# Performance work log

Measured on AMD Instinct MI355X. Metric: run time of the kernel, lower is better.

The kernel has to match this reference:

```python
import jax, jax.numpy as jnp
import numpy as np

B, T, E = 4, 2048, 1024
H, KV = 16, 4          # query heads, key/value heads
D = E // H             # head_dim = 64
G = H // KV            # query heads per kv head = 4
NEG = -1e9


def setup_inputs() -> dict:
    key = jax.random.key(0)
    ks = jax.random.split(key, 6)
    hidden_states = jax.random.normal(ks[0], (B, T, E), dtype=jnp.float32)
    # additive causal mask [B, 1, T, T]
    causal = jnp.where(jnp.tril(jnp.ones((T, T), dtype=bool)), 0.0, NEG).astype(jnp.float32)
    attention_mask = jnp.broadcast_to(causal[None, None], (B, 1, T, T))
    s = 0.02
    Wq = jax.random.normal(ks[1], (E, E), dtype=jnp.float32) * s
    Wk = jax.random.normal(ks[2], (E, KV * D), dtype=jnp.float32) * s
    Wv = jax.random.normal(ks[3], (E, KV * D), dtype=jnp.float32) * s
    Wo = jax.random.normal(ks[4], (E, E), dtype=jnp.float32) * s
    bq = jnp.zeros((E,), jnp.float32)
    bk = jnp.zeros((KV * D,), jnp.float32)
    bv = jnp.zeros((KV * D,), jnp.float32)
    bo = jnp.zeros((E,), jnp.float32)
    return {"hidden_states": hidden_states, "attention_mask": attention_mask,
            "Wq": Wq, "bq": bq, "Wk": Wk, "bk": bk, "Wv": Wv, "bv": bv,
            "Wo": Wo, "bo": bo}


def reference(hidden_states, attention_mask, Wq, bq, Wk, bk, Wv, bv, Wo, bo):
    b, t, e = hidden_states.shape
    scaling = D ** -0.5
    # projections (torch Linear: x @ W + b with W stored [in, out])
    q = (hidden_states @ Wq + bq) * scaling           # [b, t, E]
    k = hidden_states @ Wk + bk                        # [b, t, KV*D]
    v = hidden_states @ Wv + bv
    # [b, KV, G, t, D] for q; [b, KV, t, D] for k/v (GQA grouping == repeat_kv math)
    q = q.reshape(b, t, KV, G, D).transpose(0, 2, 3, 1, 4)
    k = k.reshape(b, t, KV, D).transpose(0, 2, 1, 3)
    v = v.reshape(b, t, KV, D).transpose(0, 2, 1, 3)
    scores = jnp.einsum('bkgsd,bktd->bkgst', q, k)     # [b, KV, G, t, t]
    scores = scores + attention_mask[:, :, None, :, :]  # broadcast [b,1,1,t,t]
    w = jax.nn.softmax(scores, axis=-1)
    out = jnp.einsum('bkgst,bktd->bkgsd', w, v)        # [b, KV, G, t, D]
    out = out.transpose(0, 3, 1, 2, 4).reshape(b, t, e)  # heads back to embed
    return out @ Wo + bo
```

## Files before the change

### kernel.cpp

```cpp
#include <hip/hip_runtime.h>

typedef __bf16 bf16;
typedef __attribute__((ext_vector_type(8))) __bf16 bf16x8;
typedef __attribute__((ext_vector_type(4))) __bf16 bf16x4;
typedef __attribute__((ext_vector_type(4))) float f32x4;

#define B_ 4
#define T_ 2048
#define E_ 1024
#define H_ 16
#define KV_ 4
#define D_ 64
#define KVD_ 256
#define KVSTRIDE_ 512
#define M_ 8192

#define MASK_NEG (-3.0e4f)

__device__ inline bf16x8 load8(const bf16* p) { return *(const bf16x8*)p; }
__device__ inline bf16x8 load8(const float* p) {
  f32x4 a = *(const f32x4*)p;
  f32x4 b = *(const f32x4*)(p + 4);
  bf16x8 r;
#pragma unroll
  for (int j = 0; j < 4; ++j) { r[j] = (bf16)a[j]; r[4 + j] = (bf16)b[j]; }
  return r;
}

__device__ inline void gload_lds16(const bf16* g, bf16* l) {
  __builtin_amdgcn_global_load_lds(
      (const __attribute__((address_space(1))) void*)g,
      (__attribute__((address_space(3))) void*)l, 16, 0, 0);
}

__global__ __launch_bounds__(256) void cast_k(const float* __restrict__ src,
                                              bf16* __restrict__ dst) {
  size_t i = ((size_t)blockIdx.x * 256 + threadIdx.x) * 8;
  *(bf16x8*)(dst + i) = load8(src + i);
}

__global__ __launch_bounds__(256) void transpose_k(const float* __restrict__ W,
                                                   bf16* __restrict__ WT,
                                                   int K, int N) {
  __shared__ bf16 tile[32][33];
  int k0 = blockIdx.x * 32, n0 = blockIdx.y * 32;
  int tr = threadIdx.x >> 5;
  int tc = threadIdx.x & 31;
#pragma unroll
  for (int i = 0; i < 32; i += 8)
    tile[tr + i][tc] = (bf16)W[(size_t)(k0 + tr + i) * N + n0 + tc];
  __syncthreads();
#pragma unroll
  for (int i = 0; i < 32; i += 8)
    WT[(size_t)(n0 + tr + i) * K + k0 + tc] = tile[tc][tr + i];
}

__global__ __launch_bounds__(256) void vtrans_k(const bf16* __restrict__ src,
                                                bf16* __restrict__ dst) {
  __shared__ bf16 tile[32][33];
  int r0 = blockIdx.x * 32;
  int c0 = blockIdx.y * 32;
  int tr = threadIdx.x >> 5, tc = threadIdx.x & 31;
#pragma unroll
  for (int i = 0; i < 32; i += 8)
    tile[tr + i][tc] = src[(size_t)(r0 + tr + i) * KVSTRIDE_ + 256 + c0 + tc];
  __syncthreads();
#pragma unroll
  for (int i = 0; i < 32; i += 8) {
    int c = c0 + tr + i;
    int r = r0 + tc;
    dst[(size_t)((r >> 11) * KVD_ + c) * T_ + (r & (T_ - 1))] = tile[tc][tr + i];
  }
}

template <typename CT>
__global__ __launch_bounds__(256) void gemm128_k(const bf16* __restrict__ A,
                                                 const bf16* __restrict__ WT,
                                                 const float* __restrict__ bias0,
                                                 const float* __restrict__ bias1,
                                                 int nsplit,
                                                 CT* __restrict__ C,
                                                 int M, int N, int K, float scale) {
  const int m0 = blockIdx.x * 128;
  const int n0 = blockIdx.y * 128;
  const int tid = threadIdx.x;
  const int wave = tid >> 6;
  const int lane = tid & 63;
  const int wr = wave >> 1;
  const int wc = wave & 1;
  const int fr = lane & 15;
  const int quad = lane >> 4;

  __shared__ bf16 sA[128][32];
  __shared__ bf16 sB[128][32];

  f32x4 acc[4][4] = {};

  const int ldr = lane >> 2;
  const int ldk = (lane & 3) * 8;
  const bf16* Ag0 = A + (size_t)(m0 + wave * 32 + ldr) * K + ldk;
  const bf16* Ag1 = Ag0 + (size_t)16 * K;
  const bf16* Bg0 = WT + (size_t)(n0 + wave * 32 + ldr) * K + ldk;
  const bf16* Bg1 = Bg0 + (size_t)16 * K;
  bf16* sA0 = &sA[wave * 32][0];
  bf16* sA1 = &sA[wave * 32 + 16][0];
  bf16* sB0 = &sB[wave * 32][0];
  bf16* sB1 = &sB[wave * 32 + 16][0];

  for (int k0 = 0; k0 < K; k0 += 32) {
    gload_lds16(Ag0 + k0, sA0);
    gload_lds16(Ag1 + k0, sA1);
    gload_lds16(Bg0 + k0, sB0);
    gload_lds16(Bg1 + k0, sB1);
    __syncthreads();

    bf16x8 af[4], bfr[4];
#pragma unroll
    for (int m = 0; m < 4; ++m)
      af[m] = *(const bf16x8*)(&sA[wr * 64 + m * 16 + fr][quad * 8]);
#pragma unroll
    for (int n = 0; n < 4; ++n)
      bfr[n] = *(const bf16x8*)(&sB[wc * 64 + n * 16 + fr][quad * 8]);
#pragma unroll
    for (int m = 0; m < 4; ++m)
#pragma unroll
      for (int n = 0; n < 4; ++n)
        acc[m][n] = __builtin_amdgcn_mfma_f32_16x16x32_bf16(af[m], bfr[n], acc[m][n], 0, 0, 0);
    __syncthreads();
  }

#pragma unroll
  for (int n = 0; n < 4; ++n) {
    int col = n0 + wc * 64 + n * 16 + fr;
    float bv = (col < nsplit) ? bias0[col] : bias1[col - nsplit];
#pragma unroll
    for (int m = 0; m < 4; ++m) {
#pragma unroll
      for (int i = 0; i < 4; ++i) {
        int row = m0 + wr * 64 + m * 16 + quad * 4 + i;
        C[(size_t)row * N + col] = (CT)((acc[m][n][i] + bv) * scale);
      }
    }
  }
}

__global__ __launch_bounds__(256) void attn_k(const bf16* __restrict__ Qg,
                                              const bf16* __restrict__ Kg,
                                              const bf16* __restrict__ VTg,
                                              bf16* __restrict__ Og) {
  const int jp = blockIdx.x;
  const int h = blockIdx.y;
  const int b = blockIdx.z;
  const int kv = h >> 2;
  const int tid = threadIdx.x;
  const int wave = tid >> 6;
  const int lane = tid & 63;
  const int fr = lane & 15;
  const int quad = lane >> 4;

  __shared__ bf16 Ks[64][72];
  __shared__ bf16 Vt[64][72];
  __shared__ bf16 Pt[64][72];

  const int skey = tid & 63;
  const int sdc = (tid >> 6) * 16;
  const int svd = tid >> 2;
  const int svk = (tid & 3) * 16;
  const bf16* kbase = Kg + (size_t)(b * T_ + skey) * KVSTRIDE_ + kv * 64 + sdc;
  const bf16* vbase = VTg + (size_t)((b * KV_ + kv) * D_ + svd) * T_ + svk;

  for (int ph = 0; ph < 2; ++ph) {
    const int qb = ph ? (31 - jp) : jp;

    bf16x8 qa0, qa1;
    {
      const bf16* qsrc = Qg + (size_t)(b * T_ + qb * 64 + wave * 16 + fr) * E_ + h * 64 + quad * 8;
      qa0 = *(const bf16x8*)(qsrc);
      qa1 = *(const bf16x8*)(qsrc + 32);
    }

    f32x4 Oacc[4] = {};
    float m_run = MASK_NEG, l_run = 0.f;

    bf16x8 k0p, k1p, v0p, v1p;
    k0p = *(const bf16x8*)(kbase);
    k1p = *(const bf16x8*)(kbase + 8);
    v0p = *(const bf16x8*)(vbase);
    v1p = *(const bf16x8*)(vbase + 8);

    for (int kb = 0; kb <= qb; ++kb) {
      *(bf16x8*)(&Ks[skey][sdc]) = k0p;
      *(bf16x8*)(&Ks[skey][sdc + 8]) = k1p;
      *(bf16x8*)(&Vt[svd][svk]) = v0p;
      *(bf16x8*)(&Vt[svd][svk + 8]) = v1p;
      __syncthreads();

      if (kb < qb) {
        const bf16* kp = kbase + (size_t)(kb + 1) * 64 * KVSTRIDE_;
        const bf16* vp = vbase + (size_t)(kb + 1) * 64;
        k0p = *(const bf16x8*)(kp);
        k1p = *(const bf16x8*)(kp + 8);
        v0p = *(const bf16x8*)(vp);
        v1p = *(const bf16x8*)(vp + 8);
      } else if (ph == 0) {
        k0p = *(const bf16x8*)(kbase);
        k1p = *(const bf16x8*)(kbase + 8);
        v0p = *(const bf16x8*)(vbase);
        v1p = *(const bf16x8*)(vbase + 8);
      }

      f32x4 S[4] = {};
#pragma unroll
      for (int nt = 0; nt < 4; ++nt) {
        bf16x8 kf0 = *(const bf16x8*)(&Ks[nt * 16 + fr][quad * 8]);
        bf16x8 kf1 = *(const bf16x8*)(&Ks[nt * 16 + fr][32 + quad * 8]);
        S[nt] = __builtin_amdgcn_mfma_f32_16x16x32_bf16(kf0, qa0, S[nt], 0, 0, 0);
        S[nt] = __builtin_amdgcn_mfma_f32_16x16x32_bf16(kf1, qa1, S[nt], 0, 0, 0);
      }

      if (kb == qb) {
        const int ql = wave * 16 + fr;
#pragma unroll
        for (int nt = 0; nt < 4; ++nt)
#pragma unroll
          for (int i = 0; i < 4; ++i)
            if (nt * 16 + quad * 4 + i > ql) S[nt][i] = MASK_NEG;
      }

      float pm = S[0][0];
#pragma unroll
      for (int nt = 0; nt < 4; ++nt)
#pragma unroll
        for (int i = 0; i < 4; ++i) pm = fmaxf(pm, S[nt][i]);
      pm = fmaxf(pm, __shfl_xor(pm, 16, 64));
      pm = fmaxf(pm, __shfl_xor(pm, 32, 64));
      if (pm > m_run) {
        float al = exp2f(m_run - pm);
        m_run = pm;
        l_run *= al;
#pragma unroll
        for (int dt = 0; dt < 4; ++dt)
#pragma unroll
          for (int i = 0; i < 4; ++i) Oacc[dt][i] *= al;
      }
      float ps = 0.f;
#pragma unroll
      for (int nt = 0; nt < 4; ++nt)
#pragma unroll
        for (int i = 0; i < 4; ++i) {
          float p = exp2f(S[nt][i] - m_run);
          S[nt][i] = p;
          ps += p;
        }
      ps += __shfl_xor(ps, 16, 64);
      ps += __shfl_xor(ps, 32, 64);
      l_run += ps;

#pragma unroll
      for (int nt = 0; nt < 4; ++nt) {
        bf16x4 w;
#pragma unroll
        for (int i = 0; i < 4; ++i) w[i] = (bf16)S[nt][i];
        *(bf16x4*)(&Pt[wave * 16 + fr][nt * 16 + quad * 4]) = w;
      }
      __threadfence_block();

      bf16x8 pb0 = *(const bf16x8*)(&Pt[wave * 16 + fr][quad * 8]);
      bf16x8 pb1 = *(const bf16x8*)(&Pt[wave * 16 + fr][32 + quad * 8]);
#pragma unroll
      for (int dt = 0; dt < 4; ++dt) {
        bf16x8 vf0 = *(const bf16x8*)(&Vt[dt * 16 + fr][quad * 8]);
        bf16x8 vf1 = *(const bf16x8*)(&Vt[dt * 16 + fr][32 + quad * 8]);
        Oacc[dt] = __builtin_amdgcn_mfma_f32_16x16x32_bf16(vf0, pb0, Oacc[dt], 0, 0, 0);
        Oacc[dt] = __builtin_amdgcn_mfma_f32_16x16x32_bf16(vf1, pb1, Oacc[dt], 0, 0, 0);
      }
      __syncthreads();
    }

    {
      float inv = 1.f / fmaxf(l_run, 1e-30f);
      bf16* dst = Og + (size_t)(b * T_ + qb * 64 + wave * 16 + fr) * E_ + h * 64;
#pragma unroll
      for (int dt = 0; dt < 4; ++dt) {
        bf16x4 o;
#pragma unroll
        for (int i = 0; i < 4; ++i) o[i] = (bf16)(Oacc[dt][i] * inv);
        *(bf16x4*)(dst + dt * 16 + quad * 4) = o;
      }
    }
  }
}

extern "C" void kernel_launch(void* const* d_in, const int* in_sizes, int n_in,
                              void* d_out, int out_size, void* d_ws, size_t ws_size,
                              hipStream_t stream) {
  (void)in_sizes; (void)n_in; (void)out_size; (void)ws_size;
  const float* hidden = (const float*)d_in[0];
  const float* Wq = (const float*)d_in[2];
  const float* bq = (const float*)d_in[3];
  const float* Wk = (const float*)d_in[4];
  const float* bk = (const float*)d_in[5];
  const float* Wv = (const float*)d_in[6];
  const float* bv = (const float*)d_in[7];
  const float* Wo = (const float*)d_in[8];
  const float* bo = (const float*)d_in[9];
  float* out = (float*)d_out;

  char* ws = (char*)d_ws;
  bf16* WqT  = (bf16*)(ws);
  bf16* WoT  = (bf16*)(ws + (2u << 20));
  bf16* WkvT = (bf16*)(ws + (4u << 20));
  bf16* Qb   = (bf16*)(ws + (5u << 20));
  bf16* KVb  = (bf16*)(ws + (21u << 20));
  bf16* Hb   = (bf16*)(ws + (29u << 20));
  bf16* Ab   = (bf16*)(ws + (29u << 20));
  bf16* VbT  = (bf16*)(ws + (45u << 20));

  cast_k<<<dim3(M_ * E_ / (256 * 8)), 256, 0, stream>>>(hidden, Hb);
  transpose_k<<<dim3(32, 32), 256, 0, stream>>>(Wq, WqT, 1024, 1024);
  transpose_k<<<dim3(32, 8), 256, 0, stream>>>(Wk, WkvT, 1024, 256);
  transpose_k<<<dim3(32, 8), 256, 0, stream>>>(Wv, WkvT + (256u * 1024u), 1024, 256);
  transpose_k<<<dim3(32, 32), 256, 0, stream>>>(Wo, WoT, 1024, 1024);

  gemm128_k<bf16><<<dim3(64, 8), 256, 0, stream>>>(Hb, WqT, bq, bq, 1 << 30, Qb, M_, E_, E_,
                                                   0.125f * 1.4426950408889634f);
  gemm128_k<bf16><<<dim3(64, 4), 256, 0, stream>>>(Hb, WkvT, bk, bv, 256, KVb, M_, KVSTRIDE_, E_, 1.0f);

  vtrans_k<<<dim3(256, 8), 256, 0, stream>>>(KVb, VbT);

  attn_k<<<dim3(16, 16, 4), 256, 0, stream>>>(Qb, KVb, VbT, Ab);

  gemm128_k<float><<<dim3(64, 8), 256, 0, stream>>>(Ab, WoT, bo, bo, 1 << 30, out, M_, E_, E_, 1.0f);
}
```

Before: 313.7 us.

## Fuse Q/K/V projections into one GEMM, batch weight transposes, add MFMA priority

Concatenates Wq, Wk and Wv into one transposed weight and computes Q, K and V in a single GEMM writing an interleaved QKV buffer with a 1536-column stride. The four weight transpose launches become one 3D launch. Attention and the V transpose now read from the fused buffer. The attention MFMA sections are also wrapped in s_setprio to favour matrix issue. This cuts launch count and gives better wave fill for the projections, at the cost of a wider row stride for the Q and K reads in attention.

```diff
diff --git a/kernel.cpp b/kernel.cpp
--- a/kernel.cpp
+++ b/kernel.cpp
@@ -12,10 +12,11 @@
 #define KV_ 4
 #define D_ 64
 #define KVD_ 256
-#define KVSTRIDE_ 512
+#define QKVS_ 1536
 #define M_ 8192
 
 #define MASK_NEG (-3.0e4f)
+#define QSCALE (0.125f * 1.4426950408889634f)
 
 __device__ inline bf16x8 load8(const bf16* p) { return *(const bf16x8*)p; }
 __device__ inline bf16x8 load8(const float* p) {
@@ -39,9 +40,21 @@
   *(bf16x8*)(dst + i) = load8(src + i);
 }
 
-__global__ __launch_bounds__(256) void transpose_k(const float* __restrict__ W,
-                                                   bf16* __restrict__ WT,
-                                                   int K, int N) {
+__global__ __launch_bounds__(256) void wprep_k(const float* __restrict__ Wq,
+                                               const float* __restrict__ Wk,
+                                               const float* __restrict__ Wv,
+                                               const float* __restrict__ Wo,
+                                               bf16* __restrict__ WqkvT,
+                                               bf16* __restrict__ WoT) {
+  const int z = blockIdx.z;
+  const float* W;
+  bf16* WT;
+  int N;
+  if (z == 0) { W = Wq; WT = WqkvT; N = 1024; }
+  else if (z == 1) { W = Wo; WT = WoT; N = 1024; }
+  else if (z == 2) { if (blockIdx.y >= 8) return; W = Wk; WT = WqkvT + 1024 * 1024; N = 256; }
+  else { if (blockIdx.y >= 8) return; W = Wv; WT = WqkvT + 1280 * 1024; N = 256; }
+
   __shared__ bf16 tile[32][33];
   int k0 = blockIdx.x * 32, n0 = blockIdx.y * 32;
   int tr = threadIdx.x >> 5;
@@ -52,7 +65,7 @@
   __syncthreads();
 #pragma unroll
   for (int i = 0; i < 32; i += 8)
-    WT[(size_t)(n0 + tr + i) * K + k0 + tc] = tile[tc][tr + i];
+    WT[(size_t)(n0 + tr + i) * 1024 + k0 + tc] = tile[tc][tr + i];
 }
 
 __global__ __launch_bounds__(256) void vtrans_k(const bf16* __restrict__ src,
@@ -63,7 +76,7 @@
   int tr = threadIdx.x >> 5, tc = threadIdx.x & 31;
 #pragma unroll
   for (int i = 0; i < 32; i += 8)
-    tile[tr + i][tc] = src[(size_t)(r0 + tr + i) * KVSTRIDE_ + 256 + c0 + tc];
+    tile[tr + i][tc] = src[(size_t)(r0 + tr + i) * QKVS_ + 1280 + c0 + tc];
   __syncthreads();
 #pragma unroll
   for (int i = 0; i < 32; i += 8) {
@@ -73,14 +86,13 @@
   }
 }
 
-template <typename CT>
-__global__ __launch_bounds__(256) void gemm128_k(const bf16* __restrict__ A,
-                                                 const bf16* __restrict__ WT,
-                                                 const float* __restrict__ bias0,
-                                                 const float* __restrict__ bias1,
-                                                 int nsplit,
-                                                 CT* __restrict__ C,
-                                                 int M, int N, int K, float scale) {
+__global__ __launch_bounds__(256) void qkv_gemm_k(const bf16* __restrict__ A,
+                                                  const bf16* __restrict__ WT,
+                                                  const float* __restrict__ bq,
+                                                  const float* __restrict__ bk,
+                                                  const float* __restrict__ bv,
+                                                  bf16* __restrict__ C) {
+  const int K = E_;
   const int m0 = blockIdx.x * 128;
   const int n0 = blockIdx.y * 128;
   const int tid = threadIdx.x;
@@ -132,20 +144,90 @@
 #pragma unroll
   for (int n = 0; n < 4; ++n) {
     int col = n0 + wc * 64 + n * 16 + fr;
-    float bv = (col < nsplit) ? bias0[col] : bias1[col - nsplit];
+    float bias, sc;
+    if (col < 1024) { bias = bq[col]; sc = QSCALE; }
+    else if (col < 1280) { bias = bk[col - 1024]; sc = 1.f; }
+    else { bias = bv[col - 1280]; sc = 1.f; }
 #pragma unroll
     for (int m = 0; m < 4; ++m) {
 #pragma unroll
       for (int i = 0; i < 4; ++i) {
         int row = m0 + wr * 64 + m * 16 + quad * 4 + i;
-        C[(size_t)row * N + col] = (CT)((acc[m][n][i] + bv) * scale);
+        C[(size_t)row * QKVS_ + col] = (bf16)((acc[m][n][i] + bias) * sc);
       }
     }
   }
 }
 
-__global__ __launch_bounds__(256) void attn_k(const bf16* __restrict__ Qg,
-                                              const bf16* __restrict__ Kg,
+__global__ __launch_bounds__(256) void gemm128_k(const bf16* __restrict__ A,
+                                                 const bf16* __restrict__ WT,
+                                                 const float* __restrict__ bias,
+                                                 float* __restrict__ C,
+                                                 int M, int N, int K) {
+  const int m0 = blockIdx.x * 128;
+  const int n0 = blockIdx.y * 128;
+  const int tid = threadIdx.x;
+  const int wave = tid >> 6;
+  const int lane = tid & 63;
+  const int wr = wave >> 1;
+  const int wc = wave & 1;
+  const int fr = lane & 15;
+  const int quad = lane >> 4;
+
+  __shared__ bf16 sA[128][32];
+  __shared__ bf16 sB[128][32];
+
+  f32x4 acc[4][4] = {};
+
+  const int ldr = lane >> 2;
+  const int ldk = (lane & 3) * 8;
+  const bf16* Ag0 = A + (size_t)(m0 + wave * 32 + ldr) * K + ldk;
+  const bf16* Ag1 = Ag0 + (size_t)16 * K;
+  const bf16* Bg0 = WT + (size_t)(n0 + wave * 32 + ldr) * K + ldk;
+  const bf16* Bg1 = Bg0 + (size_t)16 * K;
+  bf16* sA0 = &sA[wave * 32][0];
+  bf16* sA1 = &sA[wave * 32 + 16][0];
+  bf16* sB0 = &sB[wave * 32][0];
+  bf16* sB1 = &sB[wave * 32 + 16][0];
+
+  for (int k0 = 0; k0 < K; k0 += 32) {
+    gload_lds16(Ag0 + k0, sA0);
+    gload_lds16(Ag1 + k0, sA1);
+    gload_lds16(Bg0 + k0, sB0);
+    gload_lds16(Bg1 + k0, sB1);
+    __syncthreads();
+
+    bf16x8 af[4], bfr[4];
+#pragma unroll
+    for (int m = 0; m < 4; ++m)
+      af[m] = *(const bf16x8*)(&sA[wr * 64 + m * 16 + fr][quad * 8]);
+#pragma unroll
+    for (int n = 0; n < 4; ++n)
+      bfr[n] = *(const bf16x8*)(&sB[wc * 64 + n * 16 + fr][quad * 8]);
+#pragma unroll
+    for (int m = 0; m < 4; ++m)
+#pragma unroll
+      for (int n = 0; n < 4; ++n)
+        acc[m][n] = __builtin_amdgcn_mfma_f32_16x16x32_bf16(af[m], bfr[n], acc[m][n], 0, 0, 0);
+    __syncthreads();
+  }
+
+#pragma unroll
+  for (int n = 0; n < 4; ++n) {
+    int col = n0 + wc * 64 + n * 16 + fr;
+    float bv = bias[col];
+#pragma unroll
+    for (int m = 0; m < 4; ++m) {
+#pragma unroll
+      for (int i = 0; i < 4; ++i) {
+        int row = m0 + wr * 64 + m * 16 + quad * 4 + i;
+        C[(size_t)row * N + col] = (acc[m][n][i] + bv);
+      }
+    }
+  }
+}
+
+__global__ __launch_bounds__(256) void attn_k(const bf16* __restrict__ QKVg,
                                               const bf16* __restrict__ VTg,
                                               bf16* __restrict__ Og) {
   const int jp = blockIdx.x;
@@ -166,7 +248,7 @@
   const int sdc = (tid >> 6) * 16;
   const int svd = tid >> 2;
   const int svk = (tid & 3) * 16;
-  const bf16* kbase = Kg + (size_t)(b * T_ + skey) * KVSTRIDE_ + kv * 64 + sdc;
+  const bf16* kbase = QKVg + (size_t)(b * T_ + skey) * QKVS_ + 1024 + kv * 64 + sdc;
   const bf16* vbase = VTg + (size_t)((b * KV_ + kv) * D_ + svd) * T_ + svk;
 
   for (int ph = 0; ph < 2; ++ph) {
@@ -174,7 +256,7 @@
 
     bf16x8 qa0, qa1;
     {
-      const bf16* qsrc = Qg + (size_t)(b * T_ + qb * 64 + wave * 16 + fr) * E_ + h * 64 + quad * 8;
+      const bf16* qsrc = QKVg + (size_t)(b * T_ + qb * 64 + wave * 16 + fr) * QKVS_ + h * 64 + quad * 8;
       qa0 = *(const bf16x8*)(qsrc);
       qa1 = *(const bf16x8*)(qsrc + 32);
     }
@@ -196,7 +278,7 @@
       __syncthreads();
 
       if (kb < qb) {
-        const bf16* kp = kbase + (size_t)(kb + 1) * 64 * KVSTRIDE_;
+        const bf16* kp = kbase + (size_t)(kb + 1) * 64 * QKVS_;
         const bf16* vp = vbase + (size_t)(kb + 1) * 64;
         k0p = *(const bf16x8*)(kp);
         k1p = *(const bf16x8*)(kp + 8);
@@ -210,6 +292,7 @@
       }
 
       f32x4 S[4] = {};
+      __builtin_amdgcn_s_setprio(1);
 #pragma unroll
       for (int nt = 0; nt < 4; ++nt) {
         bf16x8 kf0 = *(const bf16x8*)(&Ks[nt * 16 + fr][quad * 8]);
@@ -217,6 +300,7 @@
         S[nt] = __builtin_amdgcn_mfma_f32_16x16x32_bf16(kf0, qa0, S[nt], 0, 0, 0);
         S[nt] = __builtin_amdgcn_mfma_f32_16x16x32_bf16(kf1, qa1, S[nt], 0, 0, 0);
       }
+      __builtin_amdgcn_s_setprio(0);
 
       if (kb == qb) {
         const int ql = wave * 16 + fr;
@@ -267,6 +351,7 @@
 
       bf16x8 pb0 = *(const bf16x8*)(&Pt[wave * 16 + fr][quad * 8]);
       bf16x8 pb1 = *(const bf16x8*)(&Pt[wave * 16 + fr][32 + quad * 8]);
+      __builtin_amdgcn_s_setprio(1);
 #pragma unroll
       for (int dt = 0; dt < 4; ++dt) {
         bf16x8 vf0 = *(const bf16x8*)(&Vt[dt * 16 + fr][quad * 8]);
@@ -274,6 +359,7 @@
         Oacc[dt] = __builtin_amdgcn_mfma_f32_16x16x32_bf16(vf0, pb0, Oacc[dt], 0, 0, 0);
         Oacc[dt] = __builtin_amdgcn_mfma_f32_16x16x32_bf16(vf1, pb1, Oacc[dt], 0, 0, 0);
       }
+      __builtin_amdgcn_s_setprio(0);
       __syncthreads();
     }
 
@@ -307,28 +393,21 @@
   float* out = (float*)d_out;
 
   char* ws = (char*)d_ws;
-  bf16* WqT  = (bf16*)(ws);
-  bf16* WoT  = (bf16*)(ws + (2u << 20));
-  bf16* WkvT = (bf16*)(ws + (4u << 20));
-  bf16* Qb   = (bf16*)(ws + (5u << 20));
-  bf16* KVb  = (bf16*)(ws + (21u << 20));
-  bf16* Hb   = (bf16*)(ws + (29u << 20));
-  bf16* Ab   = (bf16*)(ws + (29u << 20));
-  bf16* VbT  = (bf16*)(ws + (45u << 20));
+  bf16* WqkvT = (bf16*)(ws);
+  bf16* WoT   = (bf16*)(ws + (3u << 20));
+  bf16* QKVb  = (bf16*)(ws + (5u << 20));
+  bf16* Hb    = (bf16*)(ws + (29u << 20));
+  bf16* Ab    = (bf16*)(ws + (29u << 20));
+  bf16* VbT   = (bf16*)(ws + (45u << 20));
 
   cast_k<<<dim3(M_ * E_ / (256 * 8)), 256, 0, stream>>>(hidden, Hb);
-  transpose_k<<<dim3(32, 32), 256, 0, stream>>>(Wq, WqT, 1024, 1024);
-  transpose_k<<<dim3(32, 8), 256, 0, stream>>>(Wk, WkvT, 1024, 256);
-  transpose_k<<<dim3(32, 8), 256, 0, stream>>>(Wv, WkvT + (256u * 1024u), 1024, 256);
-  transpose_k<<<dim3(32, 32), 256, 0, stream>>>(Wo, WoT, 1024, 1024);
-
-  gemm128_k<bf16><<<dim3(64, 8), 256, 0, stream>>>(Hb, WqT, bq, bq, 1 << 30, Qb, M_, E_, E_,
-                                                   0.125f * 1.4426950408889634f);
-  gemm128_k<bf16><<<dim3(64, 4), 256, 0, stream>>>(Hb, WkvT, bk, bv, 256, KVb, M_, KVSTRIDE_, E_, 1.0f);
-
-  vtrans_k<<<dim3(256, 8), 256, 0, stream>>>(KVb, VbT);
-
-  attn_k<<<dim3(16, 16, 4), 256, 0, stream>>>(Qb, KVb, VbT, Ab);
-
-  gemm128_k<float><<<dim3(64, 8), 256, 0, stream>>>(Ab, WoT, bo, bo, 1 << 30, out, M_, E_, E_, 1.0f);
-}
+  wprep_k<<<dim3(32, 32, 4), 256, 0, stream>>>(Wq, Wk, Wv, Wo, WqkvT, WoT);
+
+  qkv_gemm_k<<<dim3(64, 12), 256, 0, stream>>>(Hb, WqkvT, bq, bk, bv, QKVb);
+
+  vtrans_k<<<dim3(256, 8), 256, 0, stream>>>(QKVb, VbT);
+
+  attn_k<<<dim3(16, 16, 4), 256, 0, stream>>>(QKVb, VbT, Ab);
+
+  gemm128_k<<<dim3(64, 8), 256, 0, stream>>>(Ab, WoT, bo, out, M_, E_, E_);
+}
```

Result: faster. 285.6 us (-8.9%).
